# Performance work log

Measured on AMD Instinct MI355X. Metric: run time of the kernel, lower is better.

The kernel has to match this reference:

```python
import jax, jax.numpy as jnp
import numpy as np
from jax import lax

HID = 128


def setup_inputs() -> dict:
    key = jax.random.key(0)
    ks = jax.random.split(key, 14)
    B, T, D_IN, OUT, L = 256, 300, 700, 20, 4
    x = jax.random.normal(ks[0], (B, T, D_IN), jnp.float32)
    w_in = jax.random.normal(ks[1], (D_IN, HID), jnp.float32) / np.sqrt(D_IN).astype(np.float32)
    b_in = jnp.zeros((HID,), jnp.float32)
    A_w = jax.random.normal(ks[2], (L, HID, HID), jnp.float32) / np.sqrt(HID).astype(np.float32)
    # sparse recurrent mask: keep-prob 0.3 (dropout=0.7), no self-connections
    mask = (jax.random.uniform(ks[3], (L, HID, HID)) > 0.7).astype(jnp.float32) * (1.0 - jnp.eye(HID, dtype=jnp.float32))
    A_w = A_w * mask
    A_b = jax.random.normal(ks[4], (L, HID), jnp.float32) * 0.01
    fc_w = jax.random.normal(ks[5], (L, HID, HID), jnp.float32) / np.sqrt(HID).astype(np.float32)
    fc_b = jnp.zeros((L, HID), jnp.float32)
    w_out = jax.random.normal(ks[6], (L * HID, OUT), jnp.float32) / np.sqrt(L * HID).astype(np.float32)
    b_out = jnp.zeros((OUT,), jnp.float32)
    thr = jax.random.uniform(ks[7], (HID,), jnp.float32) * 0.5
    decay = jax.random.uniform(ks[8], (HID,), jnp.float32) * 0.5
    rst = jax.random.uniform(ks[9], (HID,), jnp.float32) * 0.05
    mem0 = jax.random.uniform(ks[10], (L, B, HID), jnp.float32) * 0.1  # torch uniform_(0, 0.1)
    return dict(x=x, w_in=w_in, b_in=b_in, A_w=A_w, A_b=A_b, fc_w=fc_w, fc_b=fc_b,
                w_out=w_out, b_out=b_out, thr=thr, decay=decay, rst=rst, mem0=mem0)


def reference(x, w_in, b_in, A_w, A_b, fc_w, fc_b, w_out, b_out, thr, decay, rst, mem0):
    B, T, _ = x.shape
    # fixed input projection (fc_in frozen in original) -> [B,T,HID]
    inp = jnp.einsum('btd,dh->bth', x, w_in) + b_in
    # parallel mode: each reservoir drive depends only on input_t -> precompute all timesteps
    xs = jnp.einsum('bth,lhk->ltbk', inp, A_w) + A_b[:, None, None, :]  # [L,T,B,HID]
    xs = xs.transpose(1, 0, 2, 3)  # [T,L,B,HID]

    def step(carry, x_t):
        mem, spk = carry
        mem = rst * spk + mem * decay * (1.0 - spk) + x_t
        spike = (mem - thr > 0).astype(mem.dtype)
        return (mem, spike), (mem, spike)

    spk0 = jnp.zeros_like(mem0)
    _, (mems, spks) = lax.scan(step, (mem0, spk0), xs)  # each [T,L,B,HID]

    rates = spks.mean(axis=0)  # [L,B,HID] == sum_spk / time_step
    outs = jax.nn.relu(jnp.einsum('lbh,lhk->lbk', rates, fc_w) + fc_b[:, None, :])
    cat = jnp.concatenate([outs[0], outs[1], outs[2], outs[3]], axis=1)  # [B,4*HID]
    out = cat @ w_out + b_out  # [B,OUT]

    hid4_mem = jnp.concatenate([mem0[3][:, None, :], mems[:, 3].transpose(1, 0, 2)], axis=1)  # [B,T+1,HID]
    hid4_spk = jnp.concatenate([jnp.zeros((B, 1, HID), x.dtype), spks[:, 3].transpose(1, 0, 2)], axis=1)
    A_norm = jnp.sum(jnp.abs(A_w))
    return out, hid4_mem, hid4_spk, A_norm
```

## Files before the change

kernel.cpp:

```cpp
#include <hip/hip_runtime.h>

#define HID_   128
#define BB_    256
#define TT_    300
#define DIN_   700
#define LL_    4
#define NOUT_  20
#define NROWS_ (BB_*TT_)

#define OUT_OFF   0
#define HMEM_OFF  5120
#define HSPK_OFF  (5120 + 256*301*128)
#define ANORM_OFF (5120 + 2*256*301*128)

#define W1ELTS (22*4096)
#define A2ELTS (4*4*4096)
#define PRESPLIT_FLOATS ((2*W1ELTS + 2*A2ELTS)/2)

typedef __attribute__((ext_vector_type(8))) short  bfrag;
typedef __attribute__((ext_vector_type(4))) float  f32x4;

__device__ __forceinline__ unsigned short f2bf(float f) {
    unsigned int u = __float_as_uint(f);
    return (unsigned short)((u + 0x7fffu + ((u >> 16) & 1u)) >> 16);
}
__device__ __forceinline__ float bf2f(unsigned short h) {
    return __uint_as_float(((unsigned int)h) << 16);
}
__device__ __forceinline__ void split2(float v, unsigned short& hi, unsigned short& lo) {
    hi = f2bf(v);
    lo = f2bf(v - bf2f(hi));
}

__global__ __launch_bounds__(256)
void k0_presplit(const float* __restrict__ w, const float* __restrict__ Aw,
                 unsigned short* __restrict__ w1hi, unsigned short* __restrict__ w1lo,
                 unsigned short* __restrict__ a2hi, unsigned short* __restrict__ a2lo)
{
    const int f = blockIdx.x * 256 + threadIdx.x;
    if (f < W1ELTS) {
        const int ks = f >> 12, r = f & 4095;
        const int nt = r >> 9, l15 = (r >> 5) & 15, kk = r & 31;
        const int k = ks * 32 + kk, n = nt * 16 + l15;
        const float v = (k < DIN_) ? w[(long)k * HID_ + n] : 0.f;
        unsigned short hi, lo; split2(v, hi, lo);
        w1hi[f] = hi; w1lo[f] = lo;
    } else {
        const int g = f - W1ELTS;
        const int l = g >> 14, r2 = g & 16383;
        const int ks = r2 >> 12, r = r2 & 4095;
        const int nt = r >> 9, l15 = (r >> 5) & 15, kk = r & 31;
        const int k = ks * 32 + kk, n = nt * 16 + l15;
        const float v = Aw[(long)l * 16384 + (long)k * HID_ + n];
        unsigned short hi, lo; split2(v, hi, lo);
        a2hi[g] = hi; a2lo[g] = lo;
    }
}

__global__ __launch_bounds__(256, 2)
void k1_reg(const float* __restrict__ x,
            const unsigned short* __restrict__ whi,
            const unsigned short* __restrict__ wlo,
            const float* __restrict__ bin, float* __restrict__ inp)
{
    const int tid  = threadIdx.x;
    const int wave = tid >> 6;
    const int lane = tid & 63;
    const int l15  = lane & 15;
    const int kg   = lane >> 4;
    const long m0  = (long)blockIdx.x * 128 + wave * 32;

    f32x4 acc[2][8];
#pragma unroll
    for (int nt = 0; nt < 8; ++nt) {
        const float bv = bin[nt * 16 + l15];
        acc[0][nt] = (f32x4){bv, bv, bv, bv};
        acc[1][nt] = (f32x4){bv, bv, bv, bv};
    }

    const int foff = l15 * 32 + kg * 8;

    for (int ks = 0; ks < 22; ++ks) {
        const int kbase = ks * 32 + kg * 8;

        bfrag ahi[2], alo[2];
#pragma unroll
        for (int m = 0; m < 2; ++m) {
            const float* __restrict__ xr = x + (m0 + m * 16 + l15) * (long)DIN_ + kbase;
            if (kbase + 7 < DIN_) {
                const float4 p0 = *(const float4*)(xr);
                const float4 p1 = *(const float4*)(xr + 4);
                float vv[8] = {p0.x, p0.y, p0.z, p0.w, p1.x, p1.y, p1.z, p1.w};
#pragma unroll
                for (int j = 0; j < 8; ++j) {
                    unsigned short hi, lo; split2(vv[j], hi, lo);
                    ahi[m][j] = (short)hi; alo[m][j] = (short)lo;
                }
            } else {
#pragma unroll
                for (int j = 0; j < 8; ++j) {
                    float v = (kbase + j < DIN_) ? xr[j] : 0.f;
                    unsigned short hi, lo; split2(v, hi, lo);
                    ahi[m][j] = (short)hi; alo[m][j] = (short)lo;
                }
            }
        }

        const unsigned short* __restrict__ wh = whi + (long)ks * 4096 + foff;
        const unsigned short* __restrict__ wl = wlo + (long)ks * 4096 + foff;
#pragma unroll
        for (int nt = 0; nt < 8; ++nt) {
            const bfrag bhi = *(const bfrag*)(wh + nt * 512);
            const bfrag blo = *(const bfrag*)(wl + nt * 512);
#pragma unroll
            for (int m = 0; m < 2; ++m) {
                acc[m][nt] = __builtin_amdgcn_mfma_f32_16x16x32_bf16(ahi[m], bhi, acc[m][nt], 0, 0, 0);
                acc[m][nt] = __builtin_amdgcn_mfma_f32_16x16x32_bf16(ahi[m], blo, acc[m][nt], 0, 0, 0);
                acc[m][nt] = __builtin_amdgcn_mfma_f32_16x16x32_bf16(alo[m], bhi, acc[m][nt], 0, 0, 0);
            }
        }
    }

#pragma unroll
    for (int m = 0; m < 2; ++m)
#pragma unroll
        for (int nt = 0; nt < 8; ++nt) {
            const int col = nt * 16 + l15;
#pragma unroll
            for (int reg = 0; reg < 4; ++reg)
                inp[(m0 + m * 16 + kg * 4 + reg) * (long)HID_ + col] = acc[m][nt][reg];
        }
}

__global__ __launch_bounds__(256, 2)
void k2_reg(const float* __restrict__ inp,
            const unsigned short* __restrict__ ahiP,
            const unsigned short* __restrict__ aloP,
            const float* __restrict__ Ab, float* __restrict__ xs)
{
    const int tid  = threadIdx.x;
    const int wave = tid >> 6;
    const int lane = tid & 63;
    const int l15  = lane & 15;
    const int kg   = lane >> 4;
    const long m0  = (long)blockIdx.x * 128 + wave * 32;
    const int foff = l15 * 32 + kg * 8;

    for (int l = 0; l < 4; ++l) {
        f32x4 acc[2][8];
#pragma unroll
        for (int nt = 0; nt < 8; ++nt) {
            const float bv = Ab[l * HID_ + nt * 16 + l15];
            acc[0][nt] = (f32x4){bv, bv, bv, bv};
            acc[1][nt] = (f32x4){bv, bv, bv, bv};
        }

        const unsigned short* __restrict__ ph = ahiP + (long)l * 16384;
        const unsigned short* __restrict__ pl = aloP + (long)l * 16384;

#pragma unroll
        for (int ks = 0; ks < 4; ++ks) {
            bfrag xhi[2], xlo[2];
#pragma unroll
            for (int m = 0; m < 2; ++m) {
                const float* __restrict__ ir = inp + (m0 + m * 16 + l15) * (long)HID_ + ks * 32 + kg * 8;
                const float4 p0 = *(const float4*)(ir);
                const float4 p1 = *(const float4*)(ir + 4);
                float vv[8] = {p0.x, p0.y, p0.z, p0.w, p1.x, p1.y, p1.z, p1.w};
#pragma unroll
                for (int j = 0; j < 8; ++j) {
                    unsigned short hi, lo; split2(vv[j], hi, lo);
                    xhi[m][j] = (short)hi; xlo[m][j] = (short)lo;
                }
            }

            const unsigned short* __restrict__ bh = ph + ks * 4096 + foff;
            const unsigned short* __restrict__ bl = pl + ks * 4096 + foff;
#pragma unroll
            for (int nt = 0; nt < 8; ++nt) {
                const bfrag bhi = *(const bfrag*)(bh + nt * 512);
                const bfrag blo = *(const bfrag*)(bl + nt * 512);
#pragma unroll
                for (int m = 0; m < 2; ++m) {
                    acc[m][nt] = __builtin_amdgcn_mfma_f32_16x16x32_bf16(xhi[m], bhi, acc[m][nt], 0, 0, 0);
                    acc[m][nt] = __builtin_amdgcn_mfma_f32_16x16x32_bf16(xhi[m], blo, acc[m][nt], 0, 0, 0);
                    acc[m][nt] = __builtin_amdgcn_mfma_f32_16x16x32_bf16(xlo[m], bhi, acc[m][nt], 0, 0, 0);
                }
            }
        }

#pragma unroll
        for (int m = 0; m < 2; ++m)
#pragma unroll
            for (int nt = 0; nt < 8; ++nt) {
                const int col = nt * 16 + l15;
#pragma unroll
                for (int reg = 0; reg < 4; ++reg)
                    xs[((long)l * NROWS_ + m0 + m * 16 + kg * 4 + reg) * (long)HID_ + col] = acc[m][nt][reg];
            }
    }
}

__global__ __launch_bounds__(256, 2)
void k1_mfma(const float* __restrict__ x, const float* __restrict__ w,
             const float* __restrict__ bin, float* __restrict__ inp)
{
    __shared__ unsigned short whi[128 * 40];
    __shared__ unsigned short wlo[128 * 40];

    const int tid  = threadIdx.x;
    const int wave = tid >> 6;
    const int lane = tid & 63;
    const int l15  = lane & 15;
    const int kg   = lane >> 4;
    const long m0  = (long)blockIdx.x * 64 + wave * 16;
    const long arow = m0 + l15;

    f32x4 acc[8];
#pragma unroll
    for (int nt = 0; nt < 8; ++nt) {
        const float bv = bin[nt * 16 + l15];
        acc[nt] = (f32x4){bv, bv, bv, bv};
    }

    for (int ks = 0; ks < 22; ++ks) {
        const int k0 = ks * 32;
        const int lim = (700 - k0) * 128;
        const float* __restrict__ wsrc = w + (long)k0 * 128;
#pragma unroll
        for (int j = 0; j < 16; ++j) {
            const int i = tid + j * 256;
            const int kk = i >> 7, nn = i & 127;
            float v = (i < lim) ? wsrc[i] : 0.f;
            unsigned short hi, lo;
            split2(v, hi, lo);
            whi[nn * 40 + kk] = hi;
            wlo[nn * 40 + kk] = lo;
        }
        __syncthreads();

        bfrag ahi, alo;
        const int kbase = k0 + kg * 8;
        const float* __restrict__ xr = x + arow * (long)DIN_ + kbase;
        if (kbase + 7 < 700) {
            const float4 p0 = *(const float4*)(xr);
            const float4 p1 = *(const float4*)(xr + 4);
            float vv[8] = {p0.x, p0.y, p0.z, p0.w, p1.x, p1.y, p1.z, p1.w};
#pragma unroll
            for (int j = 0; j < 8; ++j) {
                unsigned short hi, lo; split2(vv[j], hi, lo);
                ahi[j] = (short)hi; alo[j] = (short)lo;
            }
        } else {
#pragma unroll
            for (int j = 0; j < 8; ++j) {
                float v = (kbase + j < 700) ? xr[j] : 0.f;
                unsigned short hi, lo; split2(v, hi, lo);
                ahi[j] = (short)hi; alo[j] = (short)lo;
            }
        }

#pragma unroll
        for (int nt = 0; nt < 8; ++nt) {
            const int boff = (nt * 16 + l15) * 40 + kg * 8;
            const bfrag bhi = *(const bfrag*)&whi[boff];
            const bfrag blo = *(const bfrag*)&wlo[boff];
            acc[nt] = __builtin_amdgcn_mfma_f32_16x16x32_bf16(ahi, bhi, acc[nt], 0, 0, 0);
            acc[nt] = __builtin_amdgcn_mfma_f32_16x16x32_bf16(ahi, blo, acc[nt], 0, 0, 0);
            acc[nt] = __builtin_amdgcn_mfma_f32_16x16x32_bf16(alo, bhi, acc[nt], 0, 0, 0);
        }
        __syncthreads();
    }

#pragma unroll
    for (int nt = 0; nt < 8; ++nt) {
        const int col = nt * 16 + l15;
#pragma unroll
        for (int reg = 0; reg < 4; ++reg)
            inp[(m0 + kg * 4 + reg) * (long)HID_ + col] = acc[nt][reg];
    }
}

__global__ __launch_bounds__(256, 2)
void k2_mfma(const float* __restrict__ inp, const float* __restrict__ Aw,
             const float* __restrict__ Ab, float* __restrict__ xs,
             int lsel, long lstride)
{
    __shared__ unsigned short ahiS[128 * 72];
    __shared__ unsigned short aloS[128 * 72];

    const int tid  = threadIdx.x;
    const int wave = tid >> 6;
    const int lane = tid & 63;
    const int l15  = lane & 15;
    const int kg   = lane >> 4;
    const int l    = (lsel >= 0) ? lsel : (int)blockIdx.y;
    const long m0  = (long)blockIdx.x * 64 + wave * 16;
    const long arow = m0 + l15;
    const long lbase = (lsel >= 0) ? 0 : (long)l * lstride;

    f32x4 acc[8];
#pragma unroll
    for (int nt = 0; nt < 8; ++nt) {
        const float bv = Ab[l * 128 + nt * 16 + l15];
        acc[nt] = (f32x4){bv, bv, bv, bv};
    }

    const float* __restrict__ Al = Aw + (long)l * 128 * 128;

    for (int kc = 0; kc < 2; ++kc) {
        const float* __restrict__ asrc = Al + (long)kc * 64 * 128;
#pragma unroll
        for (int j = 0; j < 32; ++j) {
            const int i = tid + j * 256;
            const int kk = i >> 7, nn = i & 127;
            unsigned short hi, lo;
            split2(asrc[i], hi, lo);
            ahiS[nn * 72 + kk] = hi;
            aloS[nn * 72 + kk] = lo;
        }
        __syncthreads();

#pragma unroll
        for (int ks = 0; ks < 2; ++ks) {
            const int k0 = kc * 64 + ks * 32;
            bfrag ahi, alo;
            const float* __restrict__ ir = inp + arow * (long)HID_ + k0 + kg * 8;
            const float4 p0 = *(const float4*)(ir);
            const float4 p1 = *(const float4*)(ir + 4);
            float vv[8] = {p0.x, p0.y, p0.z, p0.w, p1.x, p1.y, p1.z, p1.w};
#pragma unroll
            for (int j = 0; j < 8; ++j) {
                unsigned short hi, lo; split2(vv[j], hi, lo);
                ahi[j] = (short)hi; alo[j] = (short)lo;
            }

#pragma unroll
            for (int nt = 0; nt < 8; ++nt) {
                const int boff = (nt * 16 + l15) * 72 + ks * 32 + kg * 8;
                const bfrag bhi = *(const bfrag*)&ahiS[boff];
                const bfrag blo = *(const bfrag*)&aloS[boff];
                acc[nt] = __builtin_amdgcn_mfma_f32_16x16x32_bf16(ahi, bhi, acc[nt], 0, 0, 0);
                acc[nt] = __builtin_amdgcn_mfma_f32_16x16x32_bf16(ahi, blo, acc[nt], 0, 0, 0);
                acc[nt] = __builtin_amdgcn_mfma_f32_16x16x32_bf16(alo, bhi, acc[nt], 0, 0, 0);
            }
        }
        __syncthreads();
    }

#pragma unroll
    for (int nt = 0; nt < 8; ++nt) {
        const int col = nt * 16 + l15;
#pragma unroll
        for (int reg = 0; reg < 4; ++reg)
            xs[(lbase + m0 + kg * 4 + reg) * (long)HID_ + col] = acc[nt][reg];
    }
}

__global__ __launch_bounds__(128, 4)
void k3_scan_split(const float* __restrict__ xs, const float* __restrict__ thr,
                   const float* __restrict__ dec, const float* __restrict__ rstv,
                   const float* __restrict__ mem0, float* __restrict__ rates,
                   float* __restrict__ omem, float* __restrict__ ospk,
                   int lsel, long lstride)
{
    const int h = threadIdx.x;
    int l, b;
    if (lsel >= 0) { l = lsel; b = blockIdx.x; }
    else           { l = blockIdx.x >> 8; b = blockIdx.x & 255; }

    const float th = thr[h];
    const float dc = dec[h];
    const float rs = rstv[h];

    float mem = mem0[((long)l * 256 + b) * 128 + h];
    float spk = 0.f;
    float cnt = 0.f;

    const bool last = (l == 3);
    float* __restrict__ om = omem + (long)b * 301 * 128 + h;
    float* __restrict__ os = ospk + (long)b * 301 * 128 + h;
    if (last) { om[0] = mem; os[0] = 0.f; }

    const float* __restrict__ p =
        xs + ((lsel >= 0 ? 0L : (long)l * lstride) + (long)b * TT_) * HID_ + h;

    for (int t0 = 0; t0 < TT_; t0 += 20) {
        float v[20];
#pragma unroll
        for (int j = 0; j < 20; ++j) v[j] = p[(long)(t0 + j) * HID_];
#pragma unroll
        for (int j = 0; j < 20; ++j) {
            mem = rs * spk + mem * dc * (1.f - spk) + v[j];
            spk = (mem - th > 0.f) ? 1.f : 0.f;
            cnt += spk;
            if (last) {
                om[(long)(t0 + j + 1) * 128] = mem;
                os[(long)(t0 + j + 1) * 128] = spk;
            }
        }
    }

    rates[((long)l * 256 + b) * 128 + h] = cnt * (1.f / 300.f);
}

__global__ __launch_bounds__(128, 2)
void k3_fused(const float* __restrict__ inp, const float* __restrict__ Aw,
              const float* __restrict__ Ab, const float* __restrict__ thr,
              const float* __restrict__ dec, const float* __restrict__ rstv,
              const float* __restrict__ mem0, float* __restrict__ rates,
              float* __restrict__ omem, float* __restrict__ ospk)
{
    const int h = threadIdx.x;
    const int l = blockIdx.x & 3;
    const int b = blockIdx.x >> 2;

    float a[128];
#pragma unroll
    for (int k = 0; k < 128; ++k)
        a[k] = Aw[((long)l * 128 + k) * 128 + h];

    const float ab = Ab[l * 128 + h];
    const float th = thr[h];
    const float dc = dec[h];
    const float rs = rstv[h];

    float mem = mem0[((long)l * 256 + b) * 128 + h];
    float spk = 0.f, cnt = 0.f;

    const bool last = (l == 3);
    float* __restrict__ om = omem + (long)b * 301 * 128 + h;
    float* __restrict__ os = ospk + (long)b * 301 * 128 + h;
    if (last) { om[0] = mem; os[0] = 0.f; }

    const float* __restrict__ ip = inp + (long)b * 300 * 128;

    for (int t = 0; t < 300; ++t) {
        float acc = ab;
#pragma unroll
        for (int k = 0; k < 128; ++k)
            acc = fmaf(ip[k], a[k], acc);
        ip += 128;
        mem = rs * spk + mem * dc * (1.f - spk) + acc;
        spk = (mem - th > 0.f) ? 1.f : 0.f;
        cnt += spk;
        if (last) {
            om[(long)(t + 1) * 128] = mem;
            os[(long)(t + 1) * 128] = spk;
        }
    }
    rates[((long)l * 256 + b) * 128 + h] = cnt * (1.f / 300.f);
}

__global__ __launch_bounds__(256)
void k4_head(const float* __restrict__ rates, const float* __restrict__ fcw,
             const float* __restrict__ fcb, const float* __restrict__ wout,
             const float* __restrict__ bout, float* __restrict__ out)
{
    __shared__ float cat[512];
    const int b = blockIdx.x;
    const int tid = threadIdx.x;

    for (int c = tid; c < 512; c += 256) {
        const int l = c >> 7;
        const int k = c & 127;
        float s = fcb[l * 128 + k];
        const float* __restrict__ rp = rates + ((long)l * 256 + b) * 128;
        const float* __restrict__ wp = fcw + (long)l * 128 * 128 + k;
#pragma unroll 8
        for (int hh = 0; hh < 128; ++hh)
            s = fmaf(rp[hh], wp[(long)hh * 128], s);
        cat[c] = s > 0.f ? s : 0.f;
    }
    __syncthreads();

    if (tid < NOUT_) {
        float s = bout[tid];
#pragma unroll 8
        for (int c = 0; c < 512; ++c)
            s = fmaf(cat[c], wout[(long)c * NOUT_ + tid], s);
        out[(long)b * NOUT_ + tid] = s;
    }
}

__global__ __launch_bounds__(256)
void k5_anorm(const float* __restrict__ Aw, float* __restrict__ out)
{
    __shared__ float red[256];
    const int tid = threadIdx.x;
    float s = 0.f;
    for (int i = tid; i < LL_ * 128 * 128; i += 256)
        s += fabsf(Aw[i]);
    red[tid] = s;
    __syncthreads();
#pragma unroll
    for (int st = 128; st > 0; st >>= 1) {
        if (tid < st) red[tid] += red[tid + st];
        __syncthreads();
    }
    if (tid == 0) out[0] = red[0];
}

extern "C" void kernel_launch(void* const* d_in, const int* in_sizes, int n_in,
                              void* d_out, int out_size, void* d_ws, size_t ws_size,
                              hipStream_t stream)
{
    const float* x    = (const float*)d_in[0];
    const float* w_in = (const float*)d_in[1];
    const float* b_in = (const float*)d_in[2];
    const float* A_w  = (const float*)d_in[3];
    const float* A_b  = (const float*)d_in[4];
    const float* fc_w = (const float*)d_in[5];
    const float* fc_b = (const float*)d_in[6];
    const float* w_out= (const float*)d_in[7];
    const float* b_out= (const float*)d_in[8];
    const float* thr  = (const float*)d_in[9];
    const float* dec  = (const float*)d_in[10];
    const float* rst  = (const float*)d_in[11];
    const float* mem0 = (const float*)d_in[12];

    float* out = (float*)d_out;
    float* ws  = (float*)d_ws;

    const long INP_ELTS = (long)NROWS_ * HID_;
    const long XS_FULL  = 4L * NROWS_ * HID_;
    const long RATES    = 4L * 256 * 128;

    const size_t need_v2   = (size_t)(PRESPLIT_FLOATS + INP_ELTS + XS_FULL + RATES) * 4;
    const size_t need_full = (size_t)(INP_ELTS + XS_FULL + RATES) * 4;
    const size_t need_perl = (size_t)(INP_ELTS + INP_ELTS + RATES) * 4;

    if (ws_size >= need_v2) {
        unsigned short* us   = (unsigned short*)ws;
        unsigned short* w1hi = us;
        unsigned short* w1lo = us + W1ELTS;
        unsigned short* a2hi = us + 2 * W1ELTS;
        unsigned short* a2lo = us + 2 * W1ELTS + A2ELTS;
        float* inp   = ws + PRESPLIT_FLOATS;
        float* xs    = inp + INP_ELTS;
        float* rates = xs + XS_FULL;

        k0_presplit<<<608, 256, 0, stream>>>(w_in, A_w, w1hi, w1lo, a2hi, a2lo);
        k1_reg<<<600, 256, 0, stream>>>(x, w1hi, w1lo, b_in, inp);
        k2_reg<<<600, 256, 0, stream>>>(inp, a2hi, a2lo, A_b, xs);
        k3_scan_split<<<1024, 128, 0, stream>>>(xs, thr, dec, rst, mem0, rates,
                                                out + HMEM_OFF, out + HSPK_OFF,
                                                -1, (long)NROWS_);
        k4_head<<<256, 256, 0, stream>>>(rates, fc_w, fc_b, w_out, b_out, out + OUT_OFF);
    } else if (ws_size >= need_full) {
        float* inp   = ws;
        float* xs    = ws + INP_ELTS;
        float* rates = xs + XS_FULL;
        k1_mfma<<<1200, 256, 0, stream>>>(x, w_in, b_in, inp);
        k2_mfma<<<dim3(1200, 4), 256, 0, stream>>>(inp, A_w, A_b, xs, -1, (long)NROWS_);
        k3_scan_split<<<1024, 128, 0, stream>>>(xs, thr, dec, rst, mem0, rates,
                                                out + HMEM_OFF, out + HSPK_OFF,
                                                -1, (long)NROWS_);
        k4_head<<<256, 256, 0, stream>>>(rates, fc_w, fc_b, w_out, b_out, out + OUT_OFF);
    } else if (ws_size >= need_perl) {
        float* inp   = ws;
        float* xs    = ws + INP_ELTS;
        float* rates = xs + INP_ELTS;
        k1_mfma<<<1200, 256, 0, stream>>>(x, w_in, b_in, inp);
        for (int l = 0; l < 4; ++l) {
            k2_mfma<<<dim3(1200, 1), 256, 0, stream>>>(inp, A_w, A_b, xs, l, 0L);
            k3_scan_split<<<256, 128, 0, stream>>>(xs, thr, dec, rst, mem0, rates,
                                                   out + HMEM_OFF, out + HSPK_OFF,
                                                   l, 0L);
        }
        k4_head<<<256, 256, 0, stream>>>(rates, fc_w, fc_b, w_out, b_out, out + OUT_OFF);
    } else {
        float* inp   = ws;
        float* rates = ws + INP_ELTS;
        k1_mfma<<<1200, 256, 0, stream>>>(x, w_in, b_in, inp);
        k3_fused<<<1024, 128, 0, stream>>>(inp, A_w, A_b, thr, dec, rst, mem0,
                                           rates, out + HMEM_OFF, out + HSPK_OFF);
        k4_head<<<256, 256, 0, stream>>>(rates, fc_w, fc_b, w_out, b_out, out + OUT_OFF);
    }

    k5_anorm<<<1, 256, 0, stream>>>(A_w, out + ANORM_OFF);
}
```

Before: 746.4 us.

## Fuse reservoir projection GEMM with spiking scan to drop xs buffer

Merges the per-layer A_w projection and the LIF scan into one kernel: each block handles one (layer, batch) pair, computes 64-timestep chunks of the drive into shared memory with MFMA, and then 128 threads scan over them. This removes the write and re-read of the full [4,T,B,HID] xs tensor in global memory. k1 is also retiled to 16 rows per wave with higher occupancy. The cost is that half the threads sit idle during the serial scan, and each chunk adds block-wide syncs.

After: 929.6 us. 1.25x slower.

```diff
diff --git a/kernel.cpp b/kernel.cpp
--- a/kernel.cpp
+++ b/kernel.cpp
@@ -57,7 +57,7 @@
     }
 }
 
-__global__ __launch_bounds__(256, 2)
+__global__ __launch_bounds__(256, 4)
 void k1_reg(const float* __restrict__ x,
             const unsigned short* __restrict__ whi,
             const unsigned short* __restrict__ wlo,
@@ -68,14 +68,13 @@
     const int lane = tid & 63;
     const int l15  = lane & 15;
     const int kg   = lane >> 4;
-    const long m0  = (long)blockIdx.x * 128 + wave * 32;
-
-    f32x4 acc[2][8];
+    const long m0  = (long)blockIdx.x * 64 + wave * 16;
+
+    f32x4 acc[8];
 #pragma unroll
     for (int nt = 0; nt < 8; ++nt) {
         const float bv = bin[nt * 16 + l15];
-        acc[0][nt] = (f32x4){bv, bv, bv, bv};
-        acc[1][nt] = (f32x4){bv, bv, bv, bv};
+        acc[nt] = (f32x4){bv, bv, bv, bv};
     }
 
     const int foff = l15 * 32 + kg * 8;
@@ -83,26 +82,23 @@
     for (int ks = 0; ks < 22; ++ks) {
         const int kbase = ks * 32 + kg * 8;
 
-        bfrag ahi[2], alo[2];
-#pragma unroll
-        for (int m = 0; m < 2; ++m) {
-            const float* __restrict__ xr = x + (m0 + m * 16 + l15) * (long)DIN_ + kbase;
-            if (kbase + 7 < DIN_) {
-                const float4 p0 = *(const float4*)(xr);
-                const float4 p1 = *(const float4*)(xr + 4);
-                float vv[8] = {p0.x, p0.y, p0.z, p0.w, p1.x, p1.y, p1.z, p1.w};
-#pragma unroll
-                for (int j = 0; j < 8; ++j) {
-                    unsigned short hi, lo; split2(vv[j], hi, lo);
-                    ahi[m][j] = (short)hi; alo[m][j] = (short)lo;
-                }
-            } else {
-#pragma unroll
-                for (int j = 0; j < 8; ++j) {
-                    float v = (kbase + j < DIN_) ? xr[j] : 0.f;
-                    unsigned short hi, lo; split2(v, hi, lo);
-                    ahi[m][j] = (short)hi; alo[m][j] = (short)lo;
-                }
+        bfrag ahi, alo;
+        const float* __restrict__ xr = x + (m0 + l15) * (long)DIN_ + kbase;
+        if (kbase + 7 < DIN_) {
+            const float4 p0 = *(const float4*)(xr);
+            const float4 p1 = *(const float4*)(xr + 4);
+            float vv[8] = {p0.x, p0.y, p0.z, p0.w, p1.x, p1.y, p1.z, p1.w};
+#pragma unroll
+            for (int j = 0; j < 8; ++j) {
+                unsigned short hi, lo; split2(vv[j], hi, lo);
+                ahi[j] = (short)hi; alo[j] = (short)lo;
+            }
+        } else {
+#pragma unroll
+            for (int j = 0; j < 8; ++j) {
+                float v = (kbase + j < DIN_) ? xr[j] : 0.f;
+                unsigned short hi, lo; split2(v, hi, lo);
+                ahi[j] = (short)hi; alo[j] = (short)lo;
             }
         }
 
@@ -112,66 +108,81 @@
         for (int nt = 0; nt < 8; ++nt) {
             const bfrag bhi = *(const bfrag*)(wh + nt * 512);
             const bfrag blo = *(const bfrag*)(wl + nt * 512);
-#pragma unroll
-            for (int m = 0; m < 2; ++m) {
-                acc[m][nt] = __builtin_amdgcn_mfma_f32_16x16x32_bf16(ahi[m], bhi, acc[m][nt], 0, 0, 0);
-                acc[m][nt] = __builtin_amdgcn_mfma_f32_16x16x32_bf16(ahi[m], blo, acc[m][nt], 0, 0, 0);
-                acc[m][nt] = __builtin_amdgcn_mfma_f32_16x16x32_bf16(alo[m], bhi, acc[m][nt], 0, 0, 0);
-            }
-        }
-    }
-
-#pragma unroll
-    for (int m = 0; m < 2; ++m)
-#pragma unroll
-        for (int nt = 0; nt < 8; ++nt) {
-            const int col = nt * 16 + l15;
-#pragma unroll
-            for (int reg = 0; reg < 4; ++reg)
-                inp[(m0 + m * 16 + kg * 4 + reg) * (long)HID_ + col] = acc[m][nt][reg];
-        }
-}
-
-__global__ __launch_bounds__(256, 2)
-void k2_reg(const float* __restrict__ inp,
-            const unsigned short* __restrict__ ahiP,
-            const unsigned short* __restrict__ aloP,
-            const float* __restrict__ Ab, float* __restrict__ xs)
-{
+            acc[nt] = __builtin_amdgcn_mfma_f32_16x16x32_bf16(ahi, bhi, acc[nt], 0, 0, 0);
+            acc[nt] = __builtin_amdgcn_mfma_f32_16x16x32_bf16(ahi, blo, acc[nt], 0, 0, 0);
+            acc[nt] = __builtin_amdgcn_mfma_f32_16x16x32_bf16(alo, bhi, acc[nt], 0, 0, 0);
+        }
+    }
+
+#pragma unroll
+    for (int nt = 0; nt < 8; ++nt) {
+        const int col = nt * 16 + l15;
+#pragma unroll
+        for (int reg = 0; reg < 4; ++reg)
+            inp[(m0 + kg * 4 + reg) * (long)HID_ + col] = acc[nt][reg];
+    }
+}
+
+#define TC_ 64
+__global__ __launch_bounds__(256, 4)
+void k23_fused(const float* __restrict__ inp,
+               const unsigned short* __restrict__ ahiP,
+               const unsigned short* __restrict__ aloP,
+               const float* __restrict__ Ab, const float* __restrict__ thr,
+               const float* __restrict__ dec, const float* __restrict__ rstv,
+               const float* __restrict__ mem0, float* __restrict__ rates,
+               float* __restrict__ omem, float* __restrict__ ospk)
+{
+    __shared__ float xls[TC_ * 132];
+
     const int tid  = threadIdx.x;
     const int wave = tid >> 6;
     const int lane = tid & 63;
     const int l15  = lane & 15;
     const int kg   = lane >> 4;
-    const long m0  = (long)blockIdx.x * 128 + wave * 32;
+    const int bid  = blockIdx.x;
+    const int l    = bid >> 8;
+    const int b    = bid & 255;
     const int foff = l15 * 32 + kg * 8;
 
-    for (int l = 0; l < 4; ++l) {
-        f32x4 acc[2][8];
+    const unsigned short* __restrict__ ph = ahiP + (long)l * 16384;
+    const unsigned short* __restrict__ pl = aloP + (long)l * 16384;
+    const float* __restrict__ ibase = inp + (long)b * TT_ * HID_;
+
+    const int h = tid;
+    const bool isScan = (tid < 128);
+    const bool last   = (l == 3);
+    float mem = 0.f, spk = 0.f, cnt = 0.f, th = 0.f, dc = 0.f, rs = 0.f;
+    float* __restrict__ om = omem + (long)b * 301 * 128 + (h & 127);
+    float* __restrict__ os = ospk + (long)b * 301 * 128 + (h & 127);
+    if (isScan) {
+        th  = thr[h]; dc = dec[h]; rs = rstv[h];
+        mem = mem0[((long)l * 256 + b) * 128 + h];
+        if (last) { om[0] = mem; os[0] = 0.f; }
+    }
+
+    for (int t0 = 0; t0 < TT_; t0 += TC_) {
+        f32x4 acc[8];
 #pragma unroll
         for (int nt = 0; nt < 8; ++nt) {
             const float bv = Ab[l * HID_ + nt * 16 + l15];
-            acc[0][nt] = (f32x4){bv, bv, bv, bv};
-            acc[1][nt] = (f32x4){bv, bv, bv, bv};
-        }
-
-        const unsigned short* __restrict__ ph = ahiP + (long)l * 16384;
-        const unsigned short* __restrict__ pl = aloP + (long)l * 16384;
-
+            acc[nt] = (f32x4){bv, bv, bv, bv};
+        }
+
+        const int rbase = t0 + wave * 16;
 #pragma unroll
         for (int ks = 0; ks < 4; ++ks) {
-            bfrag xhi[2], xlo[2];
-#pragma unroll
-            for (int m = 0; m < 2; ++m) {
-                const float* __restrict__ ir = inp + (m0 + m * 16 + l15) * (long)HID_ + ks * 32 + kg * 8;
-                const float4 p0 = *(const float4*)(ir);
-                const float4 p1 = *(const float4*)(ir + 4);
-                float vv[8] = {p0.x, p0.y, p0.z, p0.w, p1.x, p1.y, p1.z, p1.w};
-#pragma unroll
-                for (int j = 0; j < 8; ++j) {
-                    unsigned short hi, lo; split2(vv[j], hi, lo);
-                    xhi[m][j] = (short)hi; xlo[m][j] = (short)lo;
-                }
+            int row = rbase + l15;
+            if (row > TT_ - 1) row = TT_ - 1;
+            const float* __restrict__ ir = ibase + (long)row * HID_ + ks * 32 + kg * 8;
+            const float4 p0 = *(const float4*)(ir);
+            const float4 p1 = *(const float4*)(ir + 4);
+            float vv[8] = {p0.x, p0.y, p0.z, p0.w, p1.x, p1.y, p1.z, p1.w};
+            bfrag xhi, xlo;
+#pragma unroll
+            for (int j = 0; j < 8; ++j) {
+                unsigned short hi, lo; split2(vv[j], hi, lo);
+                xhi[j] = (short)hi; xlo[j] = (short)lo;
             }
 
             const unsigned short* __restrict__ bh = ph + ks * 4096 + foff;
@@ -180,25 +191,39 @@
             for (int nt = 0; nt < 8; ++nt) {
                 const bfrag bhi = *(const bfrag*)(bh + nt * 512);
                 const bfrag blo = *(const bfrag*)(bl + nt * 512);
-#pragma unroll
-                for (int m = 0; m < 2; ++m) {
-                    acc[m][nt] = __builtin_amdgcn_mfma_f32_16x16x32_bf16(xhi[m], bhi, acc[m][nt], 0, 0, 0);
-                    acc[m][nt] = __builtin_amdgcn_mfma_f32_16x16x32_bf16(xhi[m], blo, acc[m][nt], 0, 0, 0);
-                    acc[m][nt] = __builtin_amdgcn_mfma_f32_16x16x32_bf16(xlo[m], bhi, acc[m][nt], 0, 0, 0);
+                acc[nt] = __builtin_amdgcn_mfma_f32_16x16x32_bf16(xhi, bhi, acc[nt], 0, 0, 0);
+                acc[nt] = __builtin_amdgcn_mfma_f32_16x16x32_bf16(xhi, blo, acc[nt], 0, 0, 0);
+                acc[nt] = __builtin_amdgcn_mfma_f32_16x16x32_bf16(xlo, bhi, acc[nt], 0, 0, 0);
+            }
+        }
+
+#pragma unroll
+        for (int nt = 0; nt < 8; ++nt) {
+            const int col = nt * 16 + l15;
+#pragma unroll
+            for (int reg = 0; reg < 4; ++reg)
+                xls[(wave * 16 + kg * 4 + reg) * 132 + col] = acc[nt][reg];
+        }
+        __syncthreads();
+
+        if (isScan) {
+            const int tmax = (TT_ - t0 < TC_) ? (TT_ - t0) : TC_;
+            for (int tt = 0; tt < tmax; ++tt) {
+                const float v = xls[tt * 132 + h];
+                mem = rs * spk + mem * dc * (1.f - spk) + v;
+                spk = (mem - th > 0.f) ? 1.f : 0.f;
+                cnt += spk;
+                if (last) {
+                    om[(long)(t0 + tt + 1) * 128] = mem;
+                    os[(long)(t0 + tt + 1) * 128] = spk;
                 }
             }
         }
-
-#pragma unroll
-        for (int m = 0; m < 2; ++m)
-#pragma unroll
-            for (int nt = 0; nt < 8; ++nt) {
-                const int col = nt * 16 + l15;
-#pragma unroll
-                for (int reg = 0; reg < 4; ++reg)
-                    xs[((long)l * NROWS_ + m0 + m * 16 + kg * 4 + reg) * (long)HID_ + col] = acc[m][nt][reg];
-            }
-    }
+        __syncthreads();
+    }
+
+    if (isScan)
+        rates[((long)l * 256 + b) * 128 + h] = cnt * (1.f / 300.f);
 }
 
 __global__ __launch_bounds__(256, 2)
@@ -526,26 +551,24 @@
     const long XS_FULL  = 4L * NROWS_ * HID_;
     const long RATES    = 4L * 256 * 128;
 
-    const size_t need_v2   = (size_t)(PRESPLIT_FLOATS + INP_ELTS + XS_FULL + RATES) * 4;
+    const size_t need_v3   = (size_t)(PRESPLIT_FLOATS + INP_ELTS + RATES) * 4;
     const size_t need_full = (size_t)(INP_ELTS + XS_FULL + RATES) * 4;
     const size_t need_perl = (size_t)(INP_ELTS + INP_ELTS + RATES) * 4;
 
-    if (ws_size >= need_v2) {
+    if (ws_size >= need_v3) {
         unsigned short* us   = (unsigned short*)ws;
         unsigned short* w1hi = us;
         unsigned short* w1lo = us + W1ELTS;
         unsigned short* a2hi = us + 2 * W1ELTS;
         unsigned short* a2lo = us + 2 * W1ELTS + A2ELTS;
         float* inp   = ws + PRESPLIT_FLOATS;
-        float* xs    = inp + INP_ELTS;
-        float* rates = xs + XS_FULL;
+        float* rates = inp + INP_ELTS;
 
         k0_presplit<<<608, 256, 0, stream>>>(w_in, A_w, w1hi, w1lo, a2hi, a2lo);
-        k1_reg<<<600, 256, 0, stream>>>(x, w1hi, w1lo, b_in, inp);
-        k2_reg<<<600, 256, 0, stream>>>(inp, a2hi, a2lo, A_b, xs);
-        k3_scan_split<<<1024, 128, 0, stream>>>(xs, thr, dec, rst, mem0, rates,
-                                                out + HMEM_OFF, out + HSPK_OFF,
-                                                -1, (long)NROWS_);
+        k1_reg<<<1200, 256, 0, stream>>>(x, w1hi, w1lo, b_in, inp);
+        k23_fused<<<1024, 256, 0, stream>>>(inp, a2hi, a2lo, A_b, thr, dec, rst,
+                                            mem0, rates,
+                                            out + HMEM_OFF, out + HSPK_OFF);
         k4_head<<<256, 256, 0, stream>>>(rates, fc_w, fc_b, w_out, b_out, out + OUT_OFF);
     } else if (ws_size >= need_full) {
         float* inp   = ws;
```

## Halve per-wave M tile, coalesce presplit weight layout, hoist k2 input split

Applied to the files above, without the earlier changes.

Each wave in the input-projection and reservoir-drive GEMMs now handles one 16-row tile instead of two. The launch grid doubles to 1200 blocks and launch bounds rise to 4 blocks per SIMD for more occupancy. The pre-split weight layout is reordered so each lane reads a contiguous 8-element fragment at lane*8. In k2 the split of the input rows into hi/lo bf16 is hoisted out of the layer loop, so it runs once instead of four times. The smaller tile reuses each loaded weight fragment across fewer rows, which raises weight-load traffic per FLOP.

After: 738.0 us. About the same (-1.1%).

```diff
diff --git a/kernel.cpp b/kernel.cpp
--- a/kernel.cpp
+++ b/kernel.cpp
@@ -40,8 +40,10 @@
     const int f = blockIdx.x * 256 + threadIdx.x;
     if (f < W1ELTS) {
         const int ks = f >> 12, r = f & 4095;
-        const int nt = r >> 9, l15 = (r >> 5) & 15, kk = r & 31;
-        const int k = ks * 32 + kk, n = nt * 16 + l15;
+        const int nt = r >> 9, wfl = r & 511;
+        const int lane = wfl >> 3, j = wfl & 7;
+        const int kg = lane >> 4, l15 = lane & 15;
+        const int k = ks * 32 + kg * 8 + j, n = nt * 16 + l15;
         const float v = (k < DIN_) ? w[(long)k * HID_ + n] : 0.f;
         unsigned short hi, lo; split2(v, hi, lo);
         w1hi[f] = hi; w1lo[f] = lo;
@@ -49,15 +51,17 @@
         const int g = f - W1ELTS;
         const int l = g >> 14, r2 = g & 16383;
         const int ks = r2 >> 12, r = r2 & 4095;
-        const int nt = r >> 9, l15 = (r >> 5) & 15, kk = r & 31;
-        const int k = ks * 32 + kk, n = nt * 16 + l15;
+        const int nt = r >> 9, wfl = r & 511;
+        const int lane = wfl >> 3, j = wfl & 7;
+        const int kg = lane >> 4, l15 = lane & 15;
+        const int k = ks * 32 + kg * 8 + j, n = nt * 16 + l15;
         const float v = Aw[(long)l * 16384 + (long)k * HID_ + n];
         unsigned short hi, lo; split2(v, hi, lo);
         a2hi[g] = hi; a2lo[g] = lo;
     }
 }
 
-__global__ __launch_bounds__(256, 2)
+__global__ __launch_bounds__(256, 4)
 void k1_reg(const float* __restrict__ x,
             const unsigned short* __restrict__ whi,
             const unsigned short* __restrict__ wlo,
@@ -68,41 +72,37 @@
     const int lane = tid & 63;
     const int l15  = lane & 15;
     const int kg   = lane >> 4;
-    const long m0  = (long)blockIdx.x * 128 + wave * 32;
-
-    f32x4 acc[2][8];
+    const long m0  = (long)blockIdx.x * 64 + wave * 16;
+
+    f32x4 acc[8];
 #pragma unroll
     for (int nt = 0; nt < 8; ++nt) {
         const float bv = bin[nt * 16 + l15];
-        acc[0][nt] = (f32x4){bv, bv, bv, bv};
-        acc[1][nt] = (f32x4){bv, bv, bv, bv};
-    }
-
-    const int foff = l15 * 32 + kg * 8;
+        acc[nt] = (f32x4){bv, bv, bv, bv};
+    }
+
+    const int foff = lane * 8;
 
     for (int ks = 0; ks < 22; ++ks) {
         const int kbase = ks * 32 + kg * 8;
 
-        bfrag ahi[2], alo[2];
-#pragma unroll
-        for (int m = 0; m < 2; ++m) {
-            const float* __restrict__ xr = x + (m0 + m * 16 + l15) * (long)DIN_ + kbase;
-            if (kbase + 7 < DIN_) {
-                const float4 p0 = *(const float4*)(xr);
-                const float4 p1 = *(const float4*)(xr + 4);
-                float vv[8] = {p0.x, p0.y, p0.z, p0.w, p1.x, p1.y, p1.z, p1.w};
-#pragma unroll
-                for (int j = 0; j < 8; ++j) {
-                    unsigned short hi, lo; split2(vv[j], hi, lo);
-                    ahi[m][j] = (short)hi; alo[m][j] = (short)lo;
-                }
-            } else {
-#pragma unroll
-                for (int j = 0; j < 8; ++j) {
-                    float v = (kbase + j < DIN_) ? xr[j] : 0.f;
-                    unsigned short hi, lo; split2(v, hi, lo);
-                    ahi[m][j] = (short)hi; alo[m][j] = (short)lo;
-                }
+        bfrag ahi, alo;
+        const float* __restrict__ xr = x + (m0 + l15) * (long)DIN_ + kbase;
+        if (kbase + 7 < DIN_) {
+            const float4 p0 = *(const float4*)(xr);
+            const float4 p1 = *(const float4*)(xr + 4);
+            float vv[8] = {p0.x, p0.y, p0.z, p0.w, p1.x, p1.y, p1.z, p1.w};
+#pragma unroll
+            for (int j = 0; j < 8; ++j) {
+                unsigned short hi, lo; split2(vv[j], hi, lo);
+                ahi[j] = (short)hi; alo[j] = (short)lo;
+            }
+        } else {
+#pragma unroll
+            for (int j = 0; j < 8; ++j) {
+                float v = (kbase + j < DIN_) ? xr[j] : 0.f;
+                unsigned short hi, lo; split2(v, hi, lo);
+                ahi[j] = (short)hi; alo[j] = (short)lo;
             }
         }
 
@@ -112,27 +112,22 @@
         for (int nt = 0; nt < 8; ++nt) {
             const bfrag bhi = *(const bfrag*)(wh + nt * 512);
             const bfrag blo = *(const bfrag*)(wl + nt * 512);
-#pragma unroll
-            for (int m = 0; m < 2; ++m) {
-                acc[m][nt] = __builtin_amdgcn_mfma_f32_16x16x32_bf16(ahi[m], bhi, acc[m][nt], 0, 0, 0);
-                acc[m][nt] = __builtin_amdgcn_mfma_f32_16x16x32_bf16(ahi[m], blo, acc[m][nt], 0, 0, 0);
-                acc[m][nt] = __builtin_amdgcn_mfma_f32_16x16x32_bf16(alo[m], bhi, acc[m][nt], 0, 0, 0);
-            }
-        }
-    }
-
-#pragma unroll
-    for (int m = 0; m < 2; ++m)
-#pragma unroll
-        for (int nt = 0; nt < 8; ++nt) {
-            const int col = nt * 16 + l15;
-#pragma unroll
-            for (int reg = 0; reg < 4; ++reg)
-                inp[(m0 + m * 16 + kg * 4 + reg) * (long)HID_ + col] = acc[m][nt][reg];
-        }
-}
-
-__global__ __launch_bounds__(256, 2)
+            acc[nt] = __builtin_amdgcn_mfma_f32_16x16x32_bf16(ahi, bhi, acc[nt], 0, 0, 0);
+            acc[nt] = __builtin_amdgcn_mfma_f32_16x16x32_bf16(ahi, blo, acc[nt], 0, 0, 0);
+            acc[nt] = __builtin_amdgcn_mfma_f32_16x16x32_bf16(alo, bhi, acc[nt], 0, 0, 0);
+        }
+    }
+
+#pragma unroll
+    for (int nt = 0; nt < 8; ++nt) {
+        const int col = nt * 16 + l15;
+#pragma unroll
+        for (int reg = 0; reg < 4; ++reg)
+            inp[(m0 + kg * 4 + reg) * (long)HID_ + col] = acc[nt][reg];
+    }
+}
+
+__global__ __launch_bounds__(256, 4)
 void k2_reg(const float* __restrict__ inp,
             const unsigned short* __restrict__ ahiP,
             const unsigned short* __restrict__ aloP,
@@ -143,16 +138,29 @@
     const int lane = tid & 63;
     const int l15  = lane & 15;
     const int kg   = lane >> 4;
-    const long m0  = (long)blockIdx.x * 128 + wave * 32;
-    const int foff = l15 * 32 + kg * 8;
+    const long m0  = (long)blockIdx.x * 64 + wave * 16;
+    const int foff = lane * 8;
+
+    bfrag xhi[4], xlo[4];
+#pragma unroll
+    for (int ks = 0; ks < 4; ++ks) {
+        const float* __restrict__ ir = inp + (m0 + l15) * (long)HID_ + ks * 32 + kg * 8;
+        const float4 p0 = *(const float4*)(ir);
+        const float4 p1 = *(const float4*)(ir + 4);
+        float vv[8] = {p0.x, p0.y, p0.z, p0.w, p1.x, p1.y, p1.z, p1.w};
+#pragma unroll
+        for (int j = 0; j < 8; ++j) {
+            unsigned short hi, lo; split2(vv[j], hi, lo);
+            xhi[ks][j] = (short)hi; xlo[ks][j] = (short)lo;
+        }
+    }
 
     for (int l = 0; l < 4; ++l) {
-        f32x4 acc[2][8];
+        f32x4 acc[8];
 #pragma unroll
         for (int nt = 0; nt < 8; ++nt) {
             const float bv = Ab[l * HID_ + nt * 16 + l15];
-            acc[0][nt] = (f32x4){bv, bv, bv, bv};
-            acc[1][nt] = (f32x4){bv, bv, bv, bv};
+            acc[nt] = (f32x4){bv, bv, bv, bv};
         }
 
         const unsigned short* __restrict__ ph = ahiP + (long)l * 16384;
@@ -160,44 +168,25 @@
 
 #pragma unroll
         for (int ks = 0; ks < 4; ++ks) {
-            bfrag xhi[2], xlo[2];
-#pragma unroll
-            for (int m = 0; m < 2; ++m) {
-                const float* __restrict__ ir = inp + (m0 + m * 16 + l15) * (long)HID_ + ks * 32 + kg * 8;
-                const float4 p0 = *(const float4*)(ir);
-                const float4 p1 = *(const float4*)(ir + 4);
-                float vv[8] = {p0.x, p0.y, p0.z, p0.w, p1.x, p1.y, p1.z, p1.w};
-#pragma unroll
-                for (int j = 0; j < 8; ++j) {
-                    unsigned short hi, lo; split2(vv[j], hi, lo);
-                    xhi[m][j] = (short)hi; xlo[m][j] = (short)lo;
-                }
-            }
-
             const unsigned short* __restrict__ bh = ph + ks * 4096 + foff;
             const unsigned short* __restrict__ bl = pl + ks * 4096 + foff;
 #pragma unroll
             for (int nt = 0; nt < 8; ++nt) {
                 const bfrag bhi = *(const bfrag*)(bh + nt * 512);
                 const bfrag blo = *(const bfrag*)(bl + nt * 512);
-#pragma unroll
-                for (int m = 0; m < 2; ++m) {
-                    acc[m][nt] = __builtin_amdgcn_mfma_f32_16x16x32_bf16(xhi[m], bhi, acc[m][nt], 0, 0, 0);
-                    acc[m][nt] = __builtin_amdgcn_mfma_f32_16x16x32_bf16(xhi[m], blo, acc[m][nt], 0, 0, 0);
-                    acc[m][nt] = __builtin_amdgcn_mfma_f32_16x16x32_bf16(xlo[m], bhi, acc[m][nt], 0, 0, 0);
-                }
-            }
-        }
-
-#pragma unroll
-        for (int m = 0; m < 2; ++m)
-#pragma unroll
-            for (int nt = 0; nt < 8; ++nt) {
-                const int col = nt * 16 + l15;
-#pragma unroll
-                for (int reg = 0; reg < 4; ++reg)
-                    xs[((long)l * NROWS_ + m0 + m * 16 + kg * 4 + reg) * (long)HID_ + col] = acc[m][nt][reg];
-            }
+                acc[nt] = __builtin_amdgcn_mfma_f32_16x16x32_bf16(xhi[ks], bhi, acc[nt], 0, 0, 0);
+                acc[nt] = __builtin_amdgcn_mfma_f32_16x16x32_bf16(xhi[ks], blo, acc[nt], 0, 0, 0);
+                acc[nt] = __builtin_amdgcn_mfma_f32_16x16x32_bf16(xlo[ks], bhi, acc[nt], 0, 0, 0);
+            }
+        }
+
+#pragma unroll
+        for (int nt = 0; nt < 8; ++nt) {
+            const int col = nt * 16 + l15;
+#pragma unroll
+            for (int reg = 0; reg < 4; ++reg)
+                xs[((long)l * NROWS_ + m0 + kg * 4 + reg) * (long)HID_ + col] = acc[nt][reg];
+        }
     }
 }
 
@@ -526,11 +515,11 @@
     const long XS_FULL  = 4L * NROWS_ * HID_;
     const long RATES    = 4L * 256 * 128;
 
-    const size_t need_v2   = (size_t)(PRESPLIT_FLOATS + INP_ELTS + XS_FULL + RATES) * 4;
+    const size_t need_v4   = (size_t)(PRESPLIT_FLOATS + INP_ELTS + XS_FULL + RATES) * 4;
     const size_t need_full = (size_t)(INP_ELTS + XS_FULL + RATES) * 4;
     const size_t need_perl = (size_t)(INP_ELTS + INP_ELTS + RATES) * 4;
 
-    if (ws_size >= need_v2) {
+    if (ws_size >= need_v4) {
         unsigned short* us   = (unsigned short*)ws;
         unsigned short* w1hi = us;
         unsigned short* w1lo = us + W1ELTS;
@@ -541,8 +530,8 @@
         float* rates = xs + XS_FULL;
 
         k0_presplit<<<608, 256, 0, stream>>>(w_in, A_w, w1hi, w1lo, a2hi, a2lo);
-        k1_reg<<<600, 256, 0, stream>>>(x, w1hi, w1lo, b_in, inp);
-        k2_reg<<<600, 256, 0, stream>>>(inp, a2hi, a2lo, A_b, xs);
+        k1_reg<<<1200, 256, 0, stream>>>(x, w1hi, w1lo, b_in, inp);
+        k2_reg<<<1200, 256, 0, stream>>>(inp, a2hi, a2lo, A_b, xs);
         k3_scan_split<<<1024, 128, 0, stream>>>(xs, thr, dec, rst, mem0, rates,
                                                 out + HMEM_OFF, out + HSPK_OFF,
                                                 -1, (long)NROWS_);
```
